# Kernel optimization log

Measured on AMD Instinct MI355X. Metric: run time of the kernel, lower is better.

## Reference

```python
import jax, jax.numpy as jnp
import numpy as np

TRIANGLE_TABLE = np.array([
    [-1, -1, -1, -1, -1, -1], [1, 0, 2, -1, -1, -1], [4, 0, 3, -1, -1, -1], [1, 4, 2, 1, 3, 4],
    [3, 1, 5, -1, -1, -1], [2, 3, 0, 2, 5, 3], [1, 4, 0, 1, 5, 4], [4, 2, 5, -1, -1, -1],
    [4, 5, 2, -1, -1, -1], [4, 1, 0, 4, 5, 1], [3, 2, 0, 3, 5, 2], [1, 3, 5, -1, -1, -1],
    [4, 1, 2, 4, 3, 1], [3, 0, 4, -1, -1, -1], [2, 0, 1, -1, -1, -1], [-1, -1, -1, -1, -1, -1]], np.int32)
NUM_TRIANGLES_TABLE = np.array([0, 1, 1, 2, 1, 2, 2, 1, 1, 2, 2, 1, 2, 1, 1, 0], np.int32)
BASE_TET_EDGES = np.array([0, 1, 0, 2, 0, 3, 1, 2, 1, 3, 2, 3], np.int32)


def _make_tet_grid(R):
    # Regular grid in [0,1]^3, each cube split into 6 tets along the 0-7 diagonal.
    r1 = R + 1
    gi, gj, gk = np.meshgrid(np.arange(r1), np.arange(r1), np.arange(r1), indexing='ij')
    verts = (np.stack([gi, gj, gk], -1).reshape(-1, 3) / R).astype(np.float32)  # (Nv,3)
    ci, cj, ck = np.meshgrid(np.arange(R), np.arange(R), np.arange(R), indexing='ij')
    ci, cj, ck = ci.ravel(), cj.ravel(), ck.ravel()
    def vid(dx, dy, dz):
        return ((ci + dx) * r1 + (cj + dy)) * r1 + (ck + dz)
    corners = [vid((c >> 2) & 1, (c >> 1) & 1, c & 1) for c in range(8)]
    tet_corners = [(0, 1, 3, 7), (0, 3, 2, 7), (0, 2, 6, 7), (0, 6, 4, 7), (0, 4, 5, 7), (0, 5, 1, 7)]
    tets = np.stack([np.stack([corners[a] for a in t], -1) for t in tet_corners], 1).reshape(-1, 4)
    return verts, tets.astype(np.int32)


def setup_inputs() -> dict:
    R = 64
    verts, tets = _make_tet_grid(R)
    key = jax.random.key(0)
    k1, k2 = jax.random.split(key)
    level = jax.random.normal(k1, (verts.shape[0],), dtype=jnp.float32)
    deformation = jax.random.normal(k2, (verts.shape[0], 3), dtype=jnp.float32)
    return {
        'level': level,
        'deformation': deformation,
        'grid_vertices': jnp.asarray(verts),
        'tet_indices': jnp.asarray(tets),
        'resolution': R,
    }


def reference(level, deformation, grid_vertices, tet_indices, resolution):
    # normalize_grid_deformation: (range_hi - range_lo)/res * tanh(offsets), range = (0,1)
    pos = grid_vertices + jnp.tanh(deformation) / resolution  # (Nv,3)
    occ = level > 0                                           # (Nv,)
    occ_f = occ[tet_indices]                                  # (F,4)
    occ_sum = occ_f.sum(-1)
    valid = (occ_sum > 0) & (occ_sum < 4)
    vt = tet_indices[valid]                                   # (Fv,4)
    occ_valid = occ_f[valid]                                  # (Fv,4)
    # per-tet edges, each sorted (min,max) -> dedup
    edges = vt[:, jnp.asarray(BASE_TET_EDGES)].reshape(-1, 2)  # (6*Fv,2)
    edges = jnp.sort(edges, axis=1)
    unique_edges, idx_map = jnp.unique(edges, axis=0, return_inverse=True)
    idx_map = idx_map.reshape(-1)
    # edges that actually cross the isosurface (exactly one endpoint inside)
    mask_edges = occ[unique_edges].sum(-1) == 1               # (U,)
    mapping = jnp.where(mask_edges, jnp.cumsum(mask_edges.astype(jnp.int32)) - 1, -1)
    idx_map = mapping[idx_map].reshape(-1, 6)                 # (Fv,6)
    interp_v = unique_edges[mask_edges]                       # (M,2)
    # linear interpolation of crossing point along each edge
    ep = pos[interp_v]                                        # (M,2,3)
    es = level[interp_v] * jnp.array([1.0, -1.0], dtype=level.dtype)  # (M,2) = [sdf0, -sdf1]
    w = es[:, ::-1] / es.sum(1, keepdims=True)                # (M,2) = [-sdf1, sdf0]/(sdf0-sdf1)
    verts_out = (ep * w[:, :, None]).sum(1)                   # (M,3)
    # triangle table lookup
    v_id = jnp.array([1, 2, 4, 8], dtype=jnp.int32)
    tetindex = (occ_valid.astype(jnp.int32) * v_id).sum(-1)   # (Fv,)
    tri_tab = jnp.asarray(TRIANGLE_TABLE)
    num_tri = jnp.asarray(NUM_TRIANGLES_TABLE)[tetindex]
    m1 = num_tri == 1
    m2 = num_tri == 2
    f1 = jnp.take_along_axis(idx_map[m1], tri_tab[tetindex[m1]][:, :3], axis=1).reshape(-1, 3)
    f2 = jnp.take_along_axis(idx_map[m2], tri_tab[tetindex[m2]][:, :6], axis=1).reshape(-1, 3)
    faces = jnp.concatenate([f1, f2], axis=0)                 # (Nf,3)
    return verts_out, faces
```

## Files before the change

### kernel.cpp

```cpp
#include <hip/hip_runtime.h>
#include <math.h>


typedef unsigned long long ull;

__device__ __forceinline__ float fast_tanh(float x) {
    float e = __expf(2.0f * x);
    return __fdividef(e - 1.0f, e + 1.0f);
}

__device__ __constant__ int c_tri_tab[16][6] = {
    {-1,-1,-1,-1,-1,-1},{1,0,2,-1,-1,-1},{4,0,3,-1,-1,-1},{1,4,2,1,3,4},
    {3,1,5,-1,-1,-1},{2,3,0,2,5,3},{1,4,0,1,5,4},{4,2,5,-1,-1,-1},
    {4,5,2,-1,-1,-1},{4,1,0,4,5,1},{3,2,0,3,5,2},{1,3,5,-1,-1,-1},
    {4,1,2,4,3,1},{3,0,4,-1,-1,-1},{2,0,1,-1,-1,-1},{-1,-1,-1,-1,-1,-1}};
__device__ __constant__ int c_num_tri[16] = {0,1,1,2,1,2,2,1,1,2,2,1,2,1,1,0};
__device__ __constant__ int c_tc[6][4] = {{0,1,3,7},{0,3,2,7},{0,2,6,7},{0,6,4,7},{0,4,5,7},{0,5,1,7}};
__device__ __constant__ int c_te[6][6] = {
    {(0<<3)|0,(0<<3)|2,(0<<3)|6,(1<<3)|1,(1<<3)|5,(3<<3)|3},
    {(0<<3)|2,(0<<3)|1,(0<<3)|6,(2<<3)|0,(3<<3)|3,(2<<3)|4},
    {(0<<3)|1,(0<<3)|5,(0<<3)|6,(2<<3)|3,(2<<3)|4,(6<<3)|0},
    {(0<<3)|5,(0<<3)|3,(0<<3)|6,(4<<3)|1,(6<<3)|0,(4<<3)|2},
    {(0<<3)|3,(0<<3)|4,(0<<3)|6,(4<<3)|0,(4<<3)|2,(5<<3)|1},
    {(0<<3)|4,(0<<3)|0,(0<<3)|6,(1<<3)|3,(5<<3)|1,(1<<3)|5}};

__device__ __forceinline__ void phase_a(const float* __restrict__ level, int v, int NV,
                                        int r1, int& flags, int& pk, int& ob,
                                        bool& interior, float (&lb)[7], float& la) {
    int R = r1 - 1, rsq = r1 * r1;
    flags = 0; pk = 0; ob = 0; interior = false; la = 0.f;
    if (v >= NV) return;
    la = level[v];
    bool occv = la > 0.f;
    int x = v / rsq; int rem = v - x * rsq; int y = rem / r1; int z = rem - y * r1;
    bool bx = x < R, by = y < R, bz = z < R;
    interior = bx && by && bz;
    bool inb[7] = {bz, by, by && bz, bx, bx && bz, bx && by, interior};
    int deltas[7] = {1, r1, r1 + 1, rsq, rsq + 1, rsq + r1, rsq + r1 + 1};
    ob = occv ? 1 : 0;
    for (int j = 0; j < 7; j++) {
        float l = inb[j] ? level[v + deltas[j]] : 0.f;
        lb[j] = l;
        bool o = inb[j] && (l > 0.f);
        ob |= (o ? 1 : 0) << (j + 1);
        if (inb[j] && (o != occv)) flags |= 1 << j;
    }
    if (interior) {
        int n1 = 0, n2 = 0;
        for (int k = 0; k < 6; k++) {
            int ti = ((ob >> c_tc[k][0]) & 1) | (((ob >> c_tc[k][1]) & 1) << 1)
                   | (((ob >> c_tc[k][2]) & 1) << 2) | (((ob >> c_tc[k][3]) & 1) << 3);
            int n = c_num_tri[ti];
            n1 += (n == 1); n2 += (n == 2);
        }
        pk = n1 | (n2 << 16);
    }
}

__global__ void k_count(const float* __restrict__ level, int NV, int r1,
                        ull* __restrict__ stateA) {
    int v = blockIdx.x * 256 + threadIdx.x;
    int flags, pk, ob; bool interior; float lb[7], la;
    phase_a(level, v, NV, r1, flags, pk, ob, interior, lb, la);
    int eS = __popc(flags), tS = pk;
    for (int o = 1; o < 64; o <<= 1) { eS += __shfl_xor(eS, o); tS += __shfl_xor(tS, o); }
    __shared__ int wE[4], wT[4];
    int lane = threadIdx.x & 63, wv = threadIdx.x >> 6;
    if (lane == 0) { wE[wv] = eS; wT[wv] = tS; }
    __syncthreads();
    if (threadIdx.x == 0) {
        int eb = wE[0] + wE[1] + wE[2] + wE[3];
        int tb = wT[0] + wT[1] + wT[2] + wT[3];
        stateA[blockIdx.x] = ((ull)eb << 40) | ((ull)(tb & 0xffff) << 20) | (ull)(tb >> 16);
    }
}

__global__ void k_vert(const float* __restrict__ level, const float* __restrict__ deform,
                       int NV, int r1, float invR, int nb,
                       const ull* __restrict__ stateA,
                       unsigned* __restrict__ rankWord, unsigned char* __restrict__ obByte,
                       uint2* __restrict__ cubeRank, int* __restrict__ totals,
                       float* __restrict__ out) {
    int b = blockIdx.x;
    int v = b * 256 + threadIdx.x;
    int R = r1 - 1, rsq = r1 * r1;
    int lane = threadIdx.x & 63, wv = threadIdx.x >> 6;

    int flags, pk, ob; bool interior; float lb[7], la;
    phase_a(level, v, NV, r1, flags, pk, ob, interior, lb, la);
    int cnt = __popc(flags);

    int inclE = cnt, inclT = pk;
    for (int o = 1; o < 64; o <<= 1) {
        int tE = __shfl_up(inclE, o);
        int tT = __shfl_up(inclT, o);
        if (lane >= o) { inclE += tE; inclT += tT; }
    }
    __shared__ int wE[4], wT[4];
    __shared__ ull sEx[4], sAll[4];
    if (lane == 63) { wE[wv] = inclE; wT[wv] = inclT; }

    ull sB = 0, sA = 0;
    for (int i = threadIdx.x; i < nb; i += 256) {
        ull s = stateA[i];
        sA += s;
        if (i < b) sB += s;
    }
    for (int o = 1; o < 64; o <<= 1) { sB += __shfl_xor(sB, o); sA += __shfl_xor(sA, o); }
    if (lane == 0) { sEx[wv] = sB; sAll[wv] = sA; }
    __syncthreads();
    ull exP  = sEx[0] + sEx[1] + sEx[2] + sEx[3];
    ull allP = sAll[0] + sAll[1] + sAll[2] + sAll[3];
    int exclE = (int)((exP >> 40) & 0xFFFFF);
    int excl1 = (int)((exP >> 20) & 0xFFFFF);
    int excl2 = (int)(exP & 0xFFFFF);
    if (b == 0 && threadIdx.x == 0) {
        totals[0] = (int)((allP >> 40) & 0xFFFFF);
        totals[1] = (int)((allP >> 20) & 0xFFFFF);
        totals[2] = (int)(allP & 0xFFFFF);
    }

    int woffE = 0, woffT = 0;
    for (int w = 0; w < wv; w++) { woffE += wE[w]; woffT += wT[w]; }
    int rank0 = exclE + woffE + inclE - cnt;
    int tExcl = woffT + inclT - pk;

    if (v < NV) {
        int x = v / rsq; int rem = v - x * rsq; int y = rem / r1; int z = rem - y * r1;
        if (interior) {
            int cidx = ((x * R) + y) * R + z;
            obByte[cidx] = (unsigned char)ob;
            cubeRank[cidx] = make_uint2((unsigned)(excl1 + (tExcl & 0xffff)),
                                        (unsigned)(excl2 + (tExcl >> 16)));
        }
        rankWord[v] = (unsigned)rank0 | ((unsigned)flags << 21);

        if (flags) {
            int deltas[7] = {1, r1, r1 + 1, rsq, rsq + 1, rsq + r1, rsq + r1 + 1};
            const int dxs[7] = {0, 0, 0, 1, 1, 1, 1};
            const int dys[7] = {0, 1, 1, 0, 0, 1, 1};
            const int dzs[7] = {1, 0, 1, 0, 1, 0, 1};
            float pax = x * invR + fast_tanh(deform[3 * v])     * invR;
            float pay = y * invR + fast_tanh(deform[3 * v + 1]) * invR;
            float paz = z * invR + fast_tanh(deform[3 * v + 2]) * invR;
            int r = rank0;
            for (int j = 0; j < 7; j++) {
                if (!((flags >> j) & 1)) continue;
                int bb = v + deltas[j];
                float lbv = lb[j];
                float inv = __fdividef(1.0f, la - lbv);
                float w0 = -lbv * inv;
                float w1f = la * inv;
                float pbx = (x + dxs[j]) * invR + fast_tanh(deform[3 * bb])     * invR;
                float pby = (y + dys[j]) * invR + fast_tanh(deform[3 * bb + 1]) * invR;
                float pbz = (z + dzs[j]) * invR + fast_tanh(deform[3 * bb + 2]) * invR;
                out[3 * r]     = pax * w0 + pbx * w1f;
                out[3 * r + 1] = pay * w0 + pby * w1f;
                out[3 * r + 2] = paz * w0 + pbz * w1f;
                r++;
            }
        }
    }
}

__global__ void k_face(int NV, int r1, int NT,
                       const unsigned char* __restrict__ obByte,
                       const uint2* __restrict__ cubeRank,
                       const unsigned* __restrict__ rankWord, const int* __restrict__ totals,
                       float* __restrict__ out) {
    __shared__ ull tab[256];
    if (threadIdx.x < 256) {
        int ob = threadIdx.x;
        ull w = 0;
        for (int k = 0; k < 6; k++) {
            int ti = ((ob >> c_tc[k][0]) & 1) | (((ob >> c_tc[k][1]) & 1) << 1)
                   | (((ob >> c_tc[k][2]) & 1) << 2) | (((ob >> c_tc[k][3]) & 1) << 3);
            w |= (ull)ti << (4 * k);
            w |= (ull)c_num_tri[ti] << (32 + 2 * k);
        }
        tab[ob] = w;
    }
    __syncthreads();

    int t = blockIdx.x * 256 + threadIdx.x;
    if (t >= NT) return;
    int c = t / 6;
    int k = t - c * 6;
    int ob = obByte[c];
    ull w = tab[ob];
    int nt = (int)(w >> (32 + 2 * k)) & 3;
    if (nt == 0) return;
    int ti = (int)(w >> (4 * k)) & 15;
    int pre1 = 0, pre2 = 0;
    for (int kk = 0; kk < k; kk++) {
        int m = (int)(w >> (32 + 2 * kk)) & 3;
        pre1 += (m == 1); pre2 += (m == 2);
    }
    uint2 cr = cubeRank[c];
    int R = r1 - 1, rsq = r1 * r1;
    int rr = R * R;
    int cx = c / rr; int rem = c - cx * rr; int cy = rem / R; int cz = rem - cy * R;
    int v = (cx * r1 + cy) * r1 + cz;

    int M = totals[0], N1 = totals[1];
    float* faces = out + 3 * (size_t)M;
    int off[8] = {0, 1, r1, r1 + 1, rsq, rsq + 1, rsq + r1, rsq + r1 + 1};
    int ne = nt * 3;
    float vals[6];
    for (int e = 0; e < ne; e++) {
        int le = c_tri_tab[ti][e];
        int ce = c_te[k][le];
        int a = v + off[ce >> 3];
        int j = ce & 7;
        unsigned rw = rankWord[a];
        int rk = (int)(rw & 0x1FFFFF) + __popc((rw >> 21) & (unsigned)((1 << j) - 1));
        vals[e] = (float)rk;
    }
    if (nt == 1) {
        size_t base = 3 * (size_t)(cr.x + pre1);
        faces[base] = vals[0]; faces[base + 1] = vals[1]; faces[base + 2] = vals[2];
    } else {
        size_t base = 3 * ((size_t)N1 + 2 * (size_t)(cr.y + pre2));
        for (int e = 0; e < 6; e++) faces[base + e] = vals[e];
    }
}

extern "C" void kernel_launch(void* const* d_in, const int* in_sizes, int n_in,
                              void* d_out, int out_size, void* d_ws, size_t ws_size,
                              hipStream_t stream) {
    const float* level  = (const float*)d_in[0];
    const float* deform = (const float*)d_in[1];
    int NV = in_sizes[0];
    int r1 = 1;
    while ((long long)r1 * r1 * r1 < (long long)NV) r1++;
    int R = r1 - 1;
    float invR = 1.0f / (float)R;

    int nb = (NV + 255) / 256;
    int NC = R * R * R;
    int NT = 6 * NC;
    int nbT = (NT + 255) / 256;

    char* w = (char*)d_ws;
    unsigned* rankWord = (unsigned*)w;
    w += (((size_t)NV * sizeof(unsigned)) + 255) & ~(size_t)255;
    unsigned char* obByte = (unsigned char*)w;
    w += (((size_t)NC) + 255) & ~(size_t)255;
    uint2* cubeRank = (uint2*)w;
    w += (((size_t)NC * 8) + 255) & ~(size_t)255;
    ull* stateA = (ull*)w;
    int* totals = (int*)(stateA + nb);

    float* out = (float*)d_out;

    k_count<<<nb, 256, 0, stream>>>(level, NV, r1, stateA);
    k_vert<<<nb, 256, 0, stream>>>(level, deform, NV, r1, invR, nb, stateA,
                                   rankWord, obByte, cubeRank, totals, out);
    k_face<<<nbT, 256, 0, stream>>>(NV, r1, NT, obByte, cubeRank, rankWord, totals, out);
}
```

Baseline: 130.8 us.

## Split vertex kernel into rank and per-edge emit kernels

The per-vertex classification work is now done once in k_count, which stores packed flags and triangle counts plus the occupancy byte, instead of being recomputed in the second kernel. The old vertex kernel is split into k_rank, which scans the packed words, and k_emit, which uses one thread per (vertex, edge) pair to interpolate crossing points. This removes duplicated neighbour loads and the serial, divergent per-vertex loop over up to 7 edges. In exchange it adds a kernel launch, an extra workspace buffer, and 7x more threads that mostly exit early.

```diff
diff --git a/kernel.cpp b/kernel.cpp
--- a/kernel.cpp
+++ b/kernel.cpp
@@ -24,45 +24,38 @@
     {(0<<3)|3,(0<<3)|4,(0<<3)|6,(4<<3)|0,(4<<3)|2,(5<<3)|1},
     {(0<<3)|4,(0<<3)|0,(0<<3)|6,(1<<3)|3,(5<<3)|1,(1<<3)|5}};
 
-__device__ __forceinline__ void phase_a(const float* __restrict__ level, int v, int NV,
-                                        int r1, int& flags, int& pk, int& ob,
-                                        bool& interior, float (&lb)[7], float& la) {
+__global__ void k_count(const float* __restrict__ level, int NV, int r1,
+                        ull* __restrict__ stateA, unsigned char* __restrict__ obByte,
+                        unsigned* __restrict__ pw) {
+    int v = blockIdx.x * 256 + threadIdx.x;
     int R = r1 - 1, rsq = r1 * r1;
-    flags = 0; pk = 0; ob = 0; interior = false; la = 0.f;
-    if (v >= NV) return;
-    la = level[v];
-    bool occv = la > 0.f;
-    int x = v / rsq; int rem = v - x * rsq; int y = rem / r1; int z = rem - y * r1;
-    bool bx = x < R, by = y < R, bz = z < R;
-    interior = bx && by && bz;
-    bool inb[7] = {bz, by, by && bz, bx, bx && bz, bx && by, interior};
-    int deltas[7] = {1, r1, r1 + 1, rsq, rsq + 1, rsq + r1, rsq + r1 + 1};
-    ob = occv ? 1 : 0;
-    for (int j = 0; j < 7; j++) {
-        float l = inb[j] ? level[v + deltas[j]] : 0.f;
-        lb[j] = l;
-        bool o = inb[j] && (l > 0.f);
-        ob |= (o ? 1 : 0) << (j + 1);
-        if (inb[j] && (o != occv)) flags |= 1 << j;
-    }
-    if (interior) {
-        int n1 = 0, n2 = 0;
-        for (int k = 0; k < 6; k++) {
-            int ti = ((ob >> c_tc[k][0]) & 1) | (((ob >> c_tc[k][1]) & 1) << 1)
-                   | (((ob >> c_tc[k][2]) & 1) << 2) | (((ob >> c_tc[k][3]) & 1) << 3);
-            int n = c_num_tri[ti];
-            n1 += (n == 1); n2 += (n == 2);
+    int flags = 0, n1 = 0, n2 = 0;
+    if (v < NV) {
+        float la = level[v];
+        bool occv = la > 0.f;
+        int x = v / rsq; int rem = v - x * rsq; int y = rem / r1; int z = rem - y * r1;
+        bool bx = x < R, by = y < R, bz = z < R;
+        bool interior = bx && by && bz;
+        bool inb[7] = {bz, by, by && bz, bx, bx && bz, bx && by, interior};
+        int deltas[7] = {1, r1, r1 + 1, rsq, rsq + 1, rsq + r1, rsq + r1 + 1};
+        int ob = occv ? 1 : 0;
+        for (int j = 0; j < 7; j++) {
+            bool o = inb[j] && (level[v + deltas[j]] > 0.f);
+            ob |= (o ? 1 : 0) << (j + 1);
+            if (inb[j] && (o != occv)) flags |= 1 << j;
         }
-        pk = n1 | (n2 << 16);
-    }
-}
-
-__global__ void k_count(const float* __restrict__ level, int NV, int r1,
-                        ull* __restrict__ stateA) {
-    int v = blockIdx.x * 256 + threadIdx.x;
-    int flags, pk, ob; bool interior; float lb[7], la;
-    phase_a(level, v, NV, r1, flags, pk, ob, interior, lb, la);
-    int eS = __popc(flags), tS = pk;
+        if (interior) {
+            for (int k = 0; k < 6; k++) {
+                int ti = ((ob >> c_tc[k][0]) & 1) | (((ob >> c_tc[k][1]) & 1) << 1)
+                       | (((ob >> c_tc[k][2]) & 1) << 2) | (((ob >> c_tc[k][3]) & 1) << 3);
+                int n = c_num_tri[ti];
+                n1 += (n == 1); n2 += (n == 2);
+            }
+            obByte[((x * R) + y) * R + z] = (unsigned char)ob;
+        }
+        pw[v] = (unsigned)flags | ((unsigned)n1 << 7) | ((unsigned)n2 << 10);
+    }
+    int eS = __popc(flags), tS = n1 | (n2 << 16);
     for (int o = 1; o < 64; o <<= 1) { eS += __shfl_xor(eS, o); tS += __shfl_xor(tS, o); }
     __shared__ int wE[4], wT[4];
     int lane = threadIdx.x & 63, wv = threadIdx.x >> 6;
@@ -75,20 +68,20 @@
     }
 }
 
-__global__ void k_vert(const float* __restrict__ level, const float* __restrict__ deform,
-                       int NV, int r1, float invR, int nb,
-                       const ull* __restrict__ stateA,
-                       unsigned* __restrict__ rankWord, unsigned char* __restrict__ obByte,
-                       uint2* __restrict__ cubeRank, int* __restrict__ totals,
-                       float* __restrict__ out) {
+__global__ void k_rank(int NV, int r1, int nb,
+                       const ull* __restrict__ stateA, const unsigned* __restrict__ pw,
+                       unsigned* __restrict__ rankWord, uint2* __restrict__ cubeRank,
+                       int* __restrict__ totals) {
     int b = blockIdx.x;
     int v = b * 256 + threadIdx.x;
     int R = r1 - 1, rsq = r1 * r1;
     int lane = threadIdx.x & 63, wv = threadIdx.x >> 6;
 
-    int flags, pk, ob; bool interior; float lb[7], la;
-    phase_a(level, v, NV, r1, flags, pk, ob, interior, lb, la);
+    unsigned w = (v < NV) ? pw[v] : 0u;
+    int flags = (int)(w & 127u);
+    int n1 = (int)((w >> 7) & 7u), n2 = (int)((w >> 10) & 7u);
     int cnt = __popc(flags);
+    int pk = n1 | (n2 << 16);
 
     int inclE = cnt, inclT = pk;
     for (int o = 1; o < 64; o <<= 1) {
@@ -119,48 +112,54 @@
         totals[1] = (int)((allP >> 20) & 0xFFFFF);
         totals[2] = (int)(allP & 0xFFFFF);
     }
-
     int woffE = 0, woffT = 0;
-    for (int w = 0; w < wv; w++) { woffE += wE[w]; woffT += wT[w]; }
+    for (int ww = 0; ww < wv; ww++) { woffE += wE[ww]; woffT += wT[ww]; }
     int rank0 = exclE + woffE + inclE - cnt;
     int tExcl = woffT + inclT - pk;
 
     if (v < NV) {
+        rankWord[v] = (unsigned)rank0 | ((unsigned)flags << 21);
         int x = v / rsq; int rem = v - x * rsq; int y = rem / r1; int z = rem - y * r1;
-        if (interior) {
-            int cidx = ((x * R) + y) * R + z;
-            obByte[cidx] = (unsigned char)ob;
-            cubeRank[cidx] = make_uint2((unsigned)(excl1 + (tExcl & 0xffff)),
-                                        (unsigned)(excl2 + (tExcl >> 16)));
-        }
-        rankWord[v] = (unsigned)rank0 | ((unsigned)flags << 21);
-
-        if (flags) {
-            int deltas[7] = {1, r1, r1 + 1, rsq, rsq + 1, rsq + r1, rsq + r1 + 1};
-            const int dxs[7] = {0, 0, 0, 1, 1, 1, 1};
-            const int dys[7] = {0, 1, 1, 0, 0, 1, 1};
-            const int dzs[7] = {1, 0, 1, 0, 1, 0, 1};
-            float pax = x * invR + fast_tanh(deform[3 * v])     * invR;
-            float pay = y * invR + fast_tanh(deform[3 * v + 1]) * invR;
-            float paz = z * invR + fast_tanh(deform[3 * v + 2]) * invR;
-            int r = rank0;
-            for (int j = 0; j < 7; j++) {
-                if (!((flags >> j) & 1)) continue;
-                int bb = v + deltas[j];
-                float lbv = lb[j];
-                float inv = __fdividef(1.0f, la - lbv);
-                float w0 = -lbv * inv;
-                float w1f = la * inv;
-                float pbx = (x + dxs[j]) * invR + fast_tanh(deform[3 * bb])     * invR;
-                float pby = (y + dys[j]) * invR + fast_tanh(deform[3 * bb + 1]) * invR;
-                float pbz = (z + dzs[j]) * invR + fast_tanh(deform[3 * bb + 2]) * invR;
-                out[3 * r]     = pax * w0 + pbx * w1f;
-                out[3 * r + 1] = pay * w0 + pby * w1f;
-                out[3 * r + 2] = paz * w0 + pbz * w1f;
-                r++;
-            }
-        }
-    }
+        if (x < R && y < R && z < R)
+            cubeRank[((x * R) + y) * R + z] =
+                make_uint2((unsigned)(excl1 + (tExcl & 0xffff)),
+                           (unsigned)(excl2 + (tExcl >> 16)));
+    }
+}
+
+__global__ void k_emit(const float* __restrict__ level, const float* __restrict__ deform,
+                       int NV, int r1, float invR,
+                       const unsigned* __restrict__ rankWord, float* __restrict__ out) {
+    int t = blockIdx.x * 256 + threadIdx.x;
+    if (t >= NV * 7) return;
+    int v = t / 7;
+    int j = t - v * 7;
+    unsigned rw = rankWord[v];
+    unsigned fl = rw >> 21;
+    if (!((fl >> j) & 1u)) return;
+    int rank = (int)(rw & 0x1FFFFF) + __popc(fl & ((1u << j) - 1u));
+
+    int rsq = r1 * r1;
+    int x = v / rsq; int rem = v - x * rsq; int y = rem / r1; int z = rem - y * r1;
+    const int deltas7[7] = {1, r1, r1 + 1, rsq, rsq + 1, rsq + r1, rsq + r1 + 1};
+    const int dxs[7] = {0, 0, 0, 1, 1, 1, 1};
+    const int dys[7] = {0, 1, 1, 0, 0, 1, 1};
+    const int dzs[7] = {1, 0, 1, 0, 1, 0, 1};
+    int bb = v + deltas7[j];
+    float la = level[v];
+    float lbv = level[bb];
+    float inv = __fdividef(1.0f, la - lbv);
+    float w0 = -lbv * inv;
+    float w1f = la * inv;
+    float pax = x * invR + fast_tanh(deform[3 * v])     * invR;
+    float pay = y * invR + fast_tanh(deform[3 * v + 1]) * invR;
+    float paz = z * invR + fast_tanh(deform[3 * v + 2]) * invR;
+    float pbx = (x + dxs[j]) * invR + fast_tanh(deform[3 * bb])     * invR;
+    float pby = (y + dys[j]) * invR + fast_tanh(deform[3 * bb + 1]) * invR;
+    float pbz = (z + dzs[j]) * invR + fast_tanh(deform[3 * bb + 2]) * invR;
+    out[3 * rank]     = pax * w0 + pbx * w1f;
+    out[3 * rank + 1] = pay * w0 + pby * w1f;
+    out[3 * rank + 2] = paz * w0 + pbz * w1f;
 }
 
 __global__ void k_face(int NV, int r1, int NT,
@@ -212,8 +211,8 @@
         int ce = c_te[k][le];
         int a = v + off[ce >> 3];
         int j = ce & 7;
-        unsigned rw = rankWord[a];
-        int rk = (int)(rw & 0x1FFFFF) + __popc((rw >> 21) & (unsigned)((1 << j) - 1));
+        unsigned rwv = rankWord[a];
+        int rk = (int)(rwv & 0x1FFFFF) + __popc((rwv >> 21) & (unsigned)((1 << j) - 1));
         vals[e] = (float)rk;
     }
     if (nt == 1) {
@@ -240,10 +239,13 @@
     int NC = R * R * R;
     int NT = 6 * NC;
     int nbT = (NT + 255) / 256;
+    int nbE = (NV * 7 + 255) / 256;
 
     char* w = (char*)d_ws;
     unsigned* rankWord = (unsigned*)w;
-    w += (((size_t)NV * sizeof(unsigned)) + 255) & ~(size_t)255;
+    w += (((size_t)NV * 4) + 255) & ~(size_t)255;
+    unsigned* pw = (unsigned*)w;
+    w += (((size_t)NV * 4) + 255) & ~(size_t)255;
     unsigned char* obByte = (unsigned char*)w;
     w += (((size_t)NC) + 255) & ~(size_t)255;
     uint2* cubeRank = (uint2*)w;
@@ -253,8 +255,8 @@
 
     float* out = (float*)d_out;
 
-    k_count<<<nb, 256, 0, stream>>>(level, NV, r1, stateA);
-    k_vert<<<nb, 256, 0, stream>>>(level, deform, NV, r1, invR, nb, stateA,
-                                   rankWord, obByte, cubeRank, totals, out);
+    k_count<<<nb, 256, 0, stream>>>(level, NV, r1, stateA, obByte, pw);
+    k_rank<<<nb, 256, 0, stream>>>(NV, r1, nb, stateA, pw, rankWord, cubeRank, totals);
+    k_emit<<<nbE, 256, 0, stream>>>(level, deform, NV, r1, invR, rankWord, out);
     k_face<<<nbT, 256, 0, stream>>>(NV, r1, NT, obByte, cubeRank, rankWord, totals, out);
 }
```

Result: slower. 135.9 us (+3.9%).
